# Performance work log

Hardware: AMD Instinct MI355X
Metric: run time of the kernel (lower is better)

## Reference

```python
import jax, jax.numpy as jnp
import numpy as np

B, NC, NF, D = 4, 256, 768, 768
TOK_RATIO = 0.5
LN_EPS = 1e-5


def _linear(x, w, b):
    # w: [D_in, D_out]
    return x @ w + b


def _leaky(x):
    return jax.nn.leaky_relu(x, negative_slope=0.01)


def setup_inputs() -> dict:
    key = jax.random.key(0)
    ks = jax.random.split(key, 12)
    s = 1.0 / np.sqrt(D)
    inp = {
        "cls_tokens": jax.random.normal(ks[0], (B, NC, D), dtype=jnp.float32),
        "feats": jax.random.normal(ks[1], (B, NF, D), dtype=jnp.float32),
        "W_head_w": jax.random.uniform(ks[2], (D, D), minval=-s, maxval=s),
        "W_head_b": jax.random.uniform(ks[3], (D,), minval=-s, maxval=s),
        "W_tail_w": jax.random.uniform(ks[4], (D, D), minval=-s, maxval=s),
        "W_tail_b": jax.random.uniform(ks[5], (D,), minval=-s, maxval=s),
        "lin1_w": jax.random.uniform(ks[6], (D, D), minval=-s, maxval=s),
        "lin1_b": jax.random.uniform(ks[7], (D,), minval=-s, maxval=s),
        "lin2_w": jax.random.uniform(ks[8], (D, D), minval=-s, maxval=s),
        "lin2_b": jax.random.uniform(ks[9], (D,), minval=-s, maxval=s),
        "ln_w": jnp.ones((D,), dtype=jnp.float32),
        "ln_b": jnp.zeros((D,), dtype=jnp.float32),
    }
    return inp


def reference(cls_tokens, feats, W_head_w, W_head_b, W_tail_w, W_tail_b,
              lin1_w, lin1_b, lin2_w, lin2_b, ln_w, ln_b):
    topk = int(TOK_RATIO * NC)
    scale = D ** (-0.5)

    # feats is detached in the original (clone().detach())
    x = jnp.concatenate([cls_tokens, jax.lax.stop_gradient(feats)], axis=1)  # [B, Nt, D]

    e_h = _linear(cls_tokens, W_head_w, W_head_b)  # [B, Nc, D]
    e_t = _linear(x, W_tail_w, W_tail_b)           # [B, Nt, D]

    attn_logit = jnp.einsum('bnd,bmd->bnm', e_h * scale, e_t)  # [B, Nc, Nt]
    topk_weight, topk_index = jax.lax.top_k(attn_logit, topk)  # [B, Nc, k]

    # Gather neighbor embeddings: Nb_h[b, n, j] = e_t[b, topk_index[b, n, j]]
    Nb_h = jax.vmap(lambda et, idx: et[idx])(e_t, topk_index)  # [B, Nc, k, D]

    topk_prob = jax.nn.softmax(topk_weight, axis=2)            # [B, Nc, k]
    p = topk_prob[..., None]
    eh_r = p * Nb_h + (1.0 - p) * e_h[:, :, None, :]           # [B, Nc, k, D]

    gate = jnp.tanh(e_h[:, :, None, :] + eh_r)
    ka_weight = jnp.einsum('bnkd,bnkd->bnk', Nb_h, gate)
    ka_prob = jax.nn.softmax(ka_weight, axis=2)
    e_Nh = jnp.einsum('bnk,bnkd->bnd', ka_prob, Nb_h)          # [B, Nc, D]

    # bi-interaction aggregation
    sum_emb = _leaky(_linear((e_h + e_Nh) * 0.1 + cls_tokens, lin1_w, lin1_b))
    bi_emb = _leaky(_linear(e_h * e_Nh * 0.1 + cls_tokens, lin2_w, lin2_b))
    embedding = sum_emb + bi_emb

    # LayerNorm (dropout is a no-op: p=0 and output overwritten in original)
    mu = jnp.mean(embedding, axis=-1, keepdims=True)
    var = jnp.var(embedding, axis=-1, keepdims=True)
    h = (embedding - mu) * jax.lax.rsqrt(var + LN_EPS) * ln_w + ln_b
    return h
```

## Files before the change

### kernel.cpp

```cpp
#include <hip/hip_runtime.h>
#include <hip/hip_bf16.h>
#include <math.h>

#define DDIM 768
#define NCLS 256
#define NFEAT 768
#define NTOK 1024
#define NBATCH 4
#define KSEL 128

typedef float f32x4 __attribute__((ext_vector_type(4)));
typedef short s16x8 __attribute__((ext_vector_type(8)));

__device__ __forceinline__ float wsum(float v) {
#pragma unroll
  for (int o = 32; o; o >>= 1) v += __shfl_down(v, o, 64);
  return v;
}
__device__ __forceinline__ float wmaxr(float v) {
#pragma unroll
  for (int o = 32; o; o >>= 1) v = fmaxf(v, __shfl_down(v, o, 64));
  return v;
}
__device__ __forceinline__ short f2bf(float f) {
  union { __hip_bfloat16 h; short s; } u;
  u.h = __float2bfloat16(f);
  return u.s;
}
__device__ __forceinline__ float bf2f(short s) {
  union { unsigned u; float f; } c;
  c.u = ((unsigned)(unsigned short)s) << 16;
  return c.f;
}
__device__ __forceinline__ void cvt8(float4 x, float4 y, s16x8& h, s16x8& l) {
  float v[8] = {x.x, x.y, x.z, x.w, y.x, y.y, y.z, y.w};
#pragma unroll
  for (int i = 0; i < 8; ++i) {
    short hh = f2bf(v[i]);
    h[i] = hh;
    l[i] = f2bf(v[i] - bf2f(hh));
  }
}

__global__ __launch_bounds__(256) void prep_weights(
    const float* __restrict__ w0, const float* __restrict__ w1,
    const float* __restrict__ w2, const float* __restrict__ w3,
    short* __restrict__ h0, short* __restrict__ h1, short* __restrict__ h2,
    short* __restrict__ h3, short* __restrict__ l0, short* __restrict__ l1) {
  __shared__ float tile[32][33];
  const int z = blockIdx.z;
  const float* s = z == 0 ? w0 : z == 1 ? w1 : z == 2 ? w2 : w3;
  short* dh = z == 0 ? h0 : z == 1 ? h1 : z == 2 ? h2 : h3;
  short* dl = z == 0 ? l0 : z == 1 ? l1 : nullptr;
  const int tx = threadIdx.x & 31, ty0 = threadIdx.x >> 5;
  const int r0 = blockIdx.y * 32, c0 = blockIdx.x * 32;
#pragma unroll
  for (int i = 0; i < 4; ++i) {
    int ty = ty0 + i * 8;
    tile[ty][tx] = s[(size_t)(r0 + ty) * DDIM + c0 + tx];
  }
  __syncthreads();
#pragma unroll
  for (int i = 0; i < 4; ++i) {
    int ty = ty0 + i * 8;
    float v = tile[tx][ty];
    short hh = f2bf(v);
    dh[(size_t)(c0 + ty) * DDIM + r0 + tx] = hh;
    if (dl) dl[(size_t)(c0 + ty) * DDIM + r0 + tx] = f2bf(v - bf2f(hh));
  }
}

__global__ __launch_bounds__(256) void gemm_front(
    const float* __restrict__ cls, const float* __restrict__ feats,
    const short* __restrict__ WhT_h, const short* __restrict__ WhT_l,
    const float* __restrict__ Whb, const short* __restrict__ WtT_h,
    const short* __restrict__ WtT_l, const float* __restrict__ Wtb,
    float* __restrict__ e_h, short* __restrict__ eh_hi,
    short* __restrict__ eh_lo, float* __restrict__ e_t,
    short* __restrict__ et_hi, short* __restrict__ et_lo) {
  __shared__ short Ah[64 * 40], Bh[64 * 40], Al[64 * 40], Bl[64 * 40];
  const int bid = blockIdx.x;
  const int xcd = bid & 7, idx = bid >> 3;
  const int ytile = xcd * 10 + idx / 12;
  const int xtile = idx % 12;
  const int t = threadIdx.x;
  const int row0 = ytile * 64;
  const int col0 = xtile * 64;
  const bool head = row0 < 1024;
  const int sr = t >> 2, sk = (t & 3) * 8;

  const float* aptr;
  {
    int gr = row0 + sr;
    if (head) {
      aptr = cls + (size_t)gr * DDIM;
    } else {
      int r2 = gr - 1024, b = r2 >> 10, rr = r2 & 1023;
      aptr = (rr < NCLS) ? (cls + ((size_t)b * NCLS + rr) * DDIM)
                         : (feats + ((size_t)b * NFEAT + (rr - NCLS)) * DDIM);
    }
    aptr += sk;
  }
  const short* bph = (head ? WhT_h : WtT_h) + (size_t)(col0 + sr) * DDIM + sk;
  const short* bpl = (head ? WhT_l : WtT_l) + (size_t)(col0 + sr) * DDIM + sk;
  const float* biasu = head ? Whb : Wtb;

  const int lane = t & 63, wave = t >> 6;
  const int wr = wave >> 1, wc = wave & 1;
  const int fr = lane & 15, fq = lane >> 4;

  f32x4 acc[2][2] = {};
  for (int k0 = 0; k0 < DDIM; k0 += 32) {
    float4 a0 = *(const float4*)(aptr + k0);
    float4 a1 = *(const float4*)(aptr + k0 + 4);
    s16x8 ah, al;
    cvt8(a0, a1, ah, al);
    s16x8 bh = *(const s16x8*)(bph + k0);
    s16x8 bl = *(const s16x8*)(bpl + k0);
    __syncthreads();
    *(s16x8*)&Ah[sr * 40 + sk] = ah;
    *(s16x8*)&Al[sr * 40 + sk] = al;
    *(s16x8*)&Bh[sr * 40 + sk] = bh;
    *(s16x8*)&Bl[sr * 40 + sk] = bl;
    __syncthreads();
#pragma unroll
    for (int n = 0; n < 2; ++n) {
      int bo = (wc * 32 + n * 16 + fr) * 40 + fq * 8;
      s16x8 bfh = *(const s16x8*)&Bh[bo];
      s16x8 bfl = *(const s16x8*)&Bl[bo];
#pragma unroll
      for (int m = 0; m < 2; ++m) {
        int ao = (wr * 32 + m * 16 + fr) * 40 + fq * 8;
        s16x8 afh = *(const s16x8*)&Ah[ao];
        s16x8 afl = *(const s16x8*)&Al[ao];
        acc[m][n] =
            __builtin_amdgcn_mfma_f32_16x16x32_bf16(afh, bfh, acc[m][n], 0, 0, 0);
        acc[m][n] =
            __builtin_amdgcn_mfma_f32_16x16x32_bf16(afh, bfl, acc[m][n], 0, 0, 0);
        acc[m][n] =
            __builtin_amdgcn_mfma_f32_16x16x32_bf16(afl, bfh, acc[m][n], 0, 0, 0);
      }
    }
  }

  float* Cf = head ? e_h : e_t;
  short* Ch = head ? eh_hi : et_hi;
  short* Cl = head ? eh_lo : et_lo;
  const int rbase = head ? row0 : row0 - 1024;
#pragma unroll
  for (int m = 0; m < 2; ++m) {
#pragma unroll
    for (int n = 0; n < 2; ++n) {
#pragma unroll
      for (int r = 0; r < 4; ++r) {
        int rg = rbase + wr * 32 + m * 16 + fq * 4 + r;
        int cg = col0 + wc * 32 + n * 16 + fr;
        float v = acc[m][n][r] + biasu[cg];
        size_t o = (size_t)rg * DDIM + cg;
        Cf[o] = v;
        short hh = f2bf(v);
        Ch[o] = hh;
        Cl[o] = f2bf(v - bf2f(hh));
      }
    }
  }
}

__global__ __launch_bounds__(256) void gemm_logits(
    const short* __restrict__ eh_hi, const short* __restrict__ eh_lo,
    const short* __restrict__ et_hi, const short* __restrict__ et_lo,
    float* __restrict__ logits, float scale) {
  __shared__ short Ah[32 * 40], Al[32 * 40], Bh[64 * 40], Bl[64 * 40];
  const int bid = blockIdx.x;
  const int xcd = bid & 7, idx = bid >> 3;
  const int batch = xcd >> 1;
  const int sub = ((xcd & 1) << 6) | idx;
  const int xtile = sub & 15, ytile = sub >> 4;
  const int row0 = ytile * 32, col0 = xtile * 64;
  const int t = threadIdx.x;

  const int ahalf = t >> 7, ac = t & 127;
  const int asr = ac >> 2, ask = (ac & 3) * 8;
  const short* aptr = (ahalf ? eh_lo : eh_hi) +
                      ((size_t)batch * NCLS + row0 + asr) * DDIM + ask;
  short* adst = (ahalf ? Al : Ah) + asr * 40 + ask;
  const int bsr = t >> 2, bsk = (t & 3) * 8;
  const short* bph = et_hi + ((size_t)batch * NTOK + col0 + bsr) * DDIM + bsk;
  const short* bpl = et_lo + ((size_t)batch * NTOK + col0 + bsr) * DDIM + bsk;
  short* bdh = Bh + bsr * 40 + bsk;
  short* bdl = Bl + bsr * 40 + bsk;

  const int lane = t & 63, wave = t >> 6;
  const int wr = wave >> 1, wc = wave & 1;
  const int fr = lane & 15, fq = lane >> 4;

  f32x4 acc[2] = {};
  for (int k0 = 0; k0 < DDIM; k0 += 32) {
    s16x8 av = *(const s16x8*)(aptr + k0);
    s16x8 bh = *(const s16x8*)(bph + k0);
    s16x8 bl = *(const s16x8*)(bpl + k0);
    __syncthreads();
    *(s16x8*)adst = av;
    *(s16x8*)bdh = bh;
    *(s16x8*)bdl = bl;
    __syncthreads();
    int ao = (wr * 16 + fr) * 40 + fq * 8;
    s16x8 afh = *(const s16x8*)&Ah[ao];
    s16x8 afl = *(const s16x8*)&Al[ao];
#pragma unroll
    for (int n = 0; n < 2; ++n) {
      int bo = (wc * 32 + n * 16 + fr) * 40 + fq * 8;
      s16x8 bfh = *(const s16x8*)&Bh[bo];
      s16x8 bfl = *(const s16x8*)&Bl[bo];
      acc[n] = __builtin_amdgcn_mfma_f32_16x16x32_bf16(afh, bfh, acc[n], 0, 0, 0);
      acc[n] = __builtin_amdgcn_mfma_f32_16x16x32_bf16(afh, bfl, acc[n], 0, 0, 0);
      acc[n] = __builtin_amdgcn_mfma_f32_16x16x32_bf16(afl, bfh, acc[n], 0, 0, 0);
    }
  }

  float* Cb = logits + (size_t)batch * NCLS * NTOK;
#pragma unroll
  for (int n = 0; n < 2; ++n)
#pragma unroll
    for (int r = 0; r < 4; ++r) {
      int rg = row0 + wr * 16 + fq * 4 + r;
      int cg = col0 + wc * 32 + n * 16 + fr;
      Cb[(size_t)rg * NTOK + cg] = scale * acc[n][r];
    }
}

__global__ __launch_bounds__(256) void gemm_lin(
    const short* __restrict__ inbf, const short* __restrict__ L1T,
    const short* __restrict__ L2T, const float* __restrict__ b1,
    const float* __restrict__ b2, float* __restrict__ C) {
  __shared__ short Ah[64 * 40], Bh[64 * 40];
  const int bid = blockIdx.x;
  const int xcd = bid & 7, idx = bid >> 3;
  const int ytile = xcd * 4 + idx / 12, xtile = idx % 12;
  const int t = threadIdx.x;
  const int row0 = ytile * 64, col0 = xtile * 64;
  const bool second = row0 >= 1024;
  const int sr = t >> 2, sk = (t & 3) * 8;
  const short* aptr = inbf + (size_t)(row0 + sr) * DDIM + sk;
  const short* bptr = (second ? L2T : L1T) + (size_t)(col0 + sr) * DDIM + sk;
  const float* biasu = second ? b2 : b1;
  const int lane = t & 63, wave = t >> 6;
  const int wr = wave >> 1, wc = wave & 1;
  const int fr = lane & 15, fq = lane >> 4;

  f32x4 acc[2][2] = {};
  for (int k0 = 0; k0 < DDIM; k0 += 32) {
    s16x8 ah = *(const s16x8*)(aptr + k0);
    s16x8 bh = *(const s16x8*)(bptr + k0);
    __syncthreads();
    *(s16x8*)&Ah[sr * 40 + sk] = ah;
    *(s16x8*)&Bh[sr * 40 + sk] = bh;
    __syncthreads();
#pragma unroll
    for (int n = 0; n < 2; ++n) {
      int bo = (wc * 32 + n * 16 + fr) * 40 + fq * 8;
      s16x8 bfh = *(const s16x8*)&Bh[bo];
#pragma unroll
      for (int m = 0; m < 2; ++m) {
        int ao = (wr * 32 + m * 16 + fr) * 40 + fq * 8;
        s16x8 afh = *(const s16x8*)&Ah[ao];
        acc[m][n] =
            __builtin_amdgcn_mfma_f32_16x16x32_bf16(afh, bfh, acc[m][n], 0, 0, 0);
      }
    }
  }
#pragma unroll
  for (int m = 0; m < 2; ++m)
#pragma unroll
    for (int n = 0; n < 2; ++n)
#pragma unroll
      for (int r = 0; r < 4; ++r) {
        int rg = row0 + wr * 32 + m * 16 + fq * 4 + r;
        int cg = col0 + wc * 32 + n * 16 + fr;
        float v = acc[m][n][r] + biasu[cg];
        v = v > 0.f ? v : 0.01f * v;
        C[(size_t)rg * DDIM + cg] = v;
      }
}

__global__ __launch_bounds__(256) void topk_select(
    const float* __restrict__ logits, float* __restrict__ tw,
    int* __restrict__ ti) {
  const int row = blockIdx.x;
  const int t = threadIdx.x;
  const int lane = t & 63, wave = t >> 6;
  __shared__ int hist[256];
  __shared__ int sh_bin, sh_rem;
  __shared__ int cnt;
  __shared__ int wsumT[4];

  float4 v4 = *(const float4*)(logits + (size_t)row * NTOK + 4 * t);
  float val[4] = {v4.x, v4.y, v4.z, v4.w};
  unsigned key[4];
#pragma unroll
  for (int i = 0; i < 4; ++i) {
    unsigned u = __float_as_uint(val[i]);
    key[i] = (u & 0x80000000u) ? ~u : (u | 0x80000000u);
  }

  unsigned pref = 0, mask = 0;
  int rem = KSEL;
#pragma unroll
  for (int shift = 24; shift >= 0; shift -= 8) {
    hist[t] = 0;
    __syncthreads();
#pragma unroll
    for (int i = 0; i < 4; ++i)
      if ((key[i] & mask) == pref)
        atomicAdd(&hist[(key[i] >> shift) & 255], 1);
    __syncthreads();
    if (wave == 0) {
      int h0 = hist[4 * lane], h1 = hist[4 * lane + 1];
      int h2 = hist[4 * lane + 2], h3 = hist[4 * lane + 3];
      int s = h0 + h1 + h2 + h3;
#pragma unroll
      for (int o = 1; o < 64; o <<= 1) {
        int v = __shfl_down(s, o, 64);
        if (lane + o < 64) s += v;
      }
      int abv = __shfl_down(s, 1, 64);
      if (lane == 63) abv = 0;
      int c3 = abv + h3, c2 = c3 + h2, c1 = c2 + h1, c0 = c1 + h0;
      int bin = -1, nab = 0;
      if (c3 >= rem && abv < rem) { bin = 4 * lane + 3; nab = abv; }
      else if (c2 >= rem && c3 < rem) { bin = 4 * lane + 2; nab = c3; }
      else if (c1 >= rem && c2 < rem) { bin = 4 * lane + 1; nab = c2; }
      else if (c0 >= rem && c1 < rem) { bin = 4 * lane + 0; nab = c1; }
      if (bin >= 0) { sh_bin = bin; sh_rem = rem - nab; }
    }
    __syncthreads();
    pref |= ((unsigned)sh_bin) << shift;
    mask |= 0xFFu << shift;
    rem = sh_rem;
  }

  const unsigned T = pref;
  const int above = KSEL - rem;

  if (t == 0) cnt = 0;
  int tc = 0;
#pragma unroll
  for (int i = 0; i < 4; ++i) tc += (key[i] == T);
  int inc = tc;
#pragma unroll
  for (int o = 1; o < 64; o <<= 1) {
    int v = __shfl_up(inc, o, 64);
    if (lane >= o) inc += v;
  }
  if (lane == 63) wsumT[wave] = inc;
  __syncthreads();
  int wbase = 0;
#pragma unroll
  for (int w = 0; w < 4; ++w)
    if (w < wave) wbase += wsumT[w];
  int excl = wbase + inc - tc;

  float* twr = tw + (size_t)row * KSEL;
  int* tir = ti + (size_t)row * KSEL;
#pragma unroll
  for (int i = 0; i < 4; ++i) {
    if (key[i] > T) {
      int slot = atomicAdd(&cnt, 1);
      twr[slot] = val[i];
      tir[slot] = 4 * t + i;
    } else if (key[i] == T) {
      int r = excl++;
      if (r < rem) {
        twr[above + r] = val[i];
        tir[above + r] = 4 * t + i;
      }
    }
  }
}

__global__ __launch_bounds__(256) void agg1(const float* __restrict__ e_h,
                                            const float* __restrict__ e_t,
                                            const float* __restrict__ tw,
                                            const int* __restrict__ ti,
                                            float* __restrict__ kaw_raw) {
  const int bid = blockIdx.x;
  const int xcd = bid & 7, slot = bid >> 3;
  const int batch = xcd >> 1;
  const int u = ((xcd & 1) << 8) | slot;
  const int row = batch * 256 + (u >> 1);
  const int half = u & 1;
  const int t = threadIdx.x, lane = t & 63, wave = t >> 6;
  __shared__ float p[KSEL];
  __shared__ int idxs[KSEL];
  __shared__ float red[2];

  if (t < KSEL) {
    p[t] = tw[(size_t)row * KSEL + t];
    idxs[t] = ti[(size_t)row * KSEL + t];
  }
  __syncthreads();
  if (wave == 0) {
    float m = wmaxr(fmaxf(p[lane], p[lane + 64]));
    if (!lane) red[0] = m;
  }
  __syncthreads();
  if (t < KSEL) p[t] = __expf(p[t] - red[0]);
  __syncthreads();
  if (wave == 0) {
    float s = wsum(p[lane] + p[lane + 64]);
    if (!lane) red[1] = s;
  }
  __syncthreads();
  if (t < KSEL) p[t] *= (1.f / red[1]);
  __syncthreads();

  float ehr[12];
  {
    const float* ehrow = e_h + (size_t)row * DDIM;
#pragma unroll
    for (int c = 0; c < 3; ++c) {
      float4 v = *(const float4*)(ehrow + 4 * lane + 256 * c);
      ehr[4 * c + 0] = v.x;
      ehr[4 * c + 1] = v.y;
      ehr[4 * c + 2] = v.z;
      ehr[4 * c + 3] = v.w;
    }
  }
  const float* etb = e_t + (size_t)batch * NTOK * DDIM;

  for (int i = 0; i < 16; ++i) {
    int j = half * 64 + wave * 16 + i;
    float pj = p[j];
    float a = 4.f - 2.f * pj, b2 = 2.f * pj;
    const float* nb = etb + (size_t)idxs[j] * DDIM;
    float partial = 0.f;
#pragma unroll
    for (int c = 0; c < 3; ++c) {
      float4 nv = *(const float4*)(nb + 4 * lane + 256 * c);
      float nq[4] = {nv.x, nv.y, nv.z, nv.w};
#pragma unroll
      for (int q = 0; q < 4; ++q) {
        float y2 = fmaf(a, ehr[4 * c + q], b2 * nq[q]);
        float ex = __expf(y2);
        float g = fmaf(-2.f, __builtin_amdgcn_rcpf(1.f + ex), 1.f);
        partial = fmaf(nq[q], g, partial);
      }
    }
    partial = wsum(partial);
    if (!lane) kaw_raw[(size_t)row * KSEL + j] = partial;
  }
}

__global__ __launch_bounds__(192) void agg2(
    const float* __restrict__ e_h, const float* __restrict__ e_t,
    const float* __restrict__ cls, const float* __restrict__ kaw_raw,
    const int* __restrict__ ti, short* __restrict__ inbf) {
  const int bid = blockIdx.x;
  const int xcd = bid & 7, slot = bid >> 3;
  const int batch = xcd >> 1;
  const int row = batch * 256 + (xcd & 1) * 128 + slot;
  const int t = threadIdx.x, lane = t & 63, wave = t >> 6;
  __shared__ float kp[KSEL];
  __shared__ int idxs[KSEL];
  __shared__ float red[2];

  if (t < KSEL) {
    kp[t] = kaw_raw[(size_t)row * KSEL + t];
    idxs[t] = ti[(size_t)row * KSEL + t];
  }
  __syncthreads();
  if (wave == 0) {
    float m = wmaxr(fmaxf(kp[lane], kp[lane + 64]));
    if (!lane) red[0] = m;
  }
  __syncthreads();
  if (t < KSEL) kp[t] = __expf(kp[t] - red[0]);
  __syncthreads();
  if (wave == 0) {
    float s = wsum(kp[lane] + kp[lane + 64]);
    if (!lane) red[1] = s;
  }
  __syncthreads();
  if (t < KSEL) kp[t] *= (1.f / red[1]);
  __syncthreads();

  const size_t o = (size_t)row * DDIM + 4 * t;
  float4 eh4 = *(const float4*)(e_h + o);
  float4 cl4 = *(const float4*)(cls + o);
  const float* etb = e_t + (size_t)batch * NTOK * DDIM;

  float ax = 0.f, ay = 0.f, az = 0.f, aw = 0.f;
#pragma unroll 8
  for (int j = 0; j < KSEL; ++j) {
    float pr = kp[j];
    float4 nb = *(const float4*)(etb + (size_t)idxs[j] * DDIM + 4 * t);
    ax = fmaf(pr, nb.x, ax);
    ay = fmaf(pr, nb.y, ay);
    az = fmaf(pr, nb.z, az);
    aw = fmaf(pr, nb.w, aw);
  }

  short4 sv, bv;
  sv.x = f2bf((eh4.x + ax) * 0.1f + cl4.x);
  sv.y = f2bf((eh4.y + ay) * 0.1f + cl4.y);
  sv.z = f2bf((eh4.z + az) * 0.1f + cl4.z);
  sv.w = f2bf((eh4.w + aw) * 0.1f + cl4.w);
  bv.x = f2bf((eh4.x * ax) * 0.1f + cl4.x);
  bv.y = f2bf((eh4.y * ay) * 0.1f + cl4.y);
  bv.z = f2bf((eh4.z * az) * 0.1f + cl4.z);
  bv.w = f2bf((eh4.w * aw) * 0.1f + cl4.w);
  *(short4*)&inbf[o] = sv;
  *(short4*)&inbf[(size_t)(NBATCH * NCLS) * DDIM + o] = bv;
}

__global__ __launch_bounds__(256) void ln_kernel(const float* __restrict__ embA,
                                                 const float* __restrict__ embB,
                                                 const float* __restrict__ lw,
                                                 const float* __restrict__ lb,
                                                 float* __restrict__ out) {
  const int row = blockIdx.x;
  const int t = threadIdx.x;
  const int lane = t & 63, wave = t >> 6;
  __shared__ float red[4];
  __shared__ float bs[2];
  float e[3];
#pragma unroll
  for (int c = 0; c < 3; ++c) {
    size_t o = (size_t)row * DDIM + t + 256 * c;
    e[c] = embA[o] + embB[o];
  }
  float s = e[0] + e[1] + e[2];
  s = wsum(s);
  if (lane == 0) red[wave] = s;
  __syncthreads();
  if (t == 0) bs[0] = (red[0] + red[1] + red[2] + red[3]) * (1.f / DDIM);
  __syncthreads();
  float mu = bs[0];
  float q = 0.f;
#pragma unroll
  for (int c = 0; c < 3; ++c) {
    float d = e[c] - mu;
    q = fmaf(d, d, q);
  }
  q = wsum(q);
  if (lane == 0) red[wave] = q;
  __syncthreads();
  if (t == 0) bs[1] = (red[0] + red[1] + red[2] + red[3]) * (1.f / DDIM);
  __syncthreads();
  float rstd = rsqrtf(bs[1] + 1e-5f);
#pragma unroll
  for (int c = 0; c < 3; ++c) {
    int d = t + 256 * c;
    out[(size_t)row * DDIM + d] = (e[c] - mu) * rstd * lw[d] + lb[d];
  }
}

extern "C" void kernel_launch(void* const* d_in, const int* in_sizes, int n_in,
                              void* d_out, int out_size, void* d_ws,
                              size_t ws_size, hipStream_t stream) {
  const float* cls = (const float*)d_in[0];
  const float* feats = (const float*)d_in[1];
  const float* Whw = (const float*)d_in[2];
  const float* Whb = (const float*)d_in[3];
  const float* Wtw = (const float*)d_in[4];
  const float* Wtb = (const float*)d_in[5];
  const float* l1w = (const float*)d_in[6];
  const float* l1b = (const float*)d_in[7];
  const float* l2w = (const float*)d_in[8];
  const float* l2b = (const float*)d_in[9];
  const float* lnw = (const float*)d_in[10];
  const float* lnb = (const float*)d_in[11];
  float* out = (float*)d_out;

  float* ws = (float*)d_ws;
  float* e_h = ws;
  float* e_t = ws + 786432;
  short* eh_hi = (short*)(ws + 3932160);
  short* eh_lo = eh_hi + 786432;
  short* et_hi = (short*)(ws + 4718592);
  short* et_lo = et_hi + 3145728;
  short* WhT_h = (short*)(ws + 7864320);
  short* WhT_l = WhT_h + 589824;
  short* WtT_h = WhT_h + 2 * 589824;
  short* WtT_l = WhT_h + 3 * 589824;
  short* L1T = (short*)(ws + 9043968);
  short* L2T = L1T + 589824;
  float* logits = ws + 7864320;
  float* tw = ws + 9633792;
  int* ti = (int*)(ws + 9764864);
  float* kaw = ws + 9895936;
  short* inbf = (short*)(ws + 10027008);
  float* linC = e_t;
  (void)ws_size;
  (void)in_sizes;
  (void)n_in;
  (void)out_size;

  const float scale = 0.036084391824351615f;
  dim3 blk(256);

  prep_weights<<<dim3(24, 24, 4), blk, 0, stream>>>(
      Whw, Wtw, l1w, l2w, WhT_h, WtT_h, L1T, L2T, WhT_l, WtT_l);
  gemm_front<<<dim3(960), blk, 0, stream>>>(
      cls, feats, WhT_h, WhT_l, Whb, WtT_h, WtT_l, Wtb, e_h, eh_hi, eh_lo, e_t,
      et_hi, et_lo);
  gemm_logits<<<dim3(512), blk, 0, stream>>>(eh_hi, eh_lo, et_hi, et_lo,
                                             logits, scale);
  topk_select<<<dim3(NBATCH * NCLS), blk, 0, stream>>>(logits, tw, ti);
  agg1<<<dim3(2048), blk, 0, stream>>>(e_h, e_t, tw, ti, kaw);
  agg2<<<dim3(1024), dim3(192), 0, stream>>>(e_h, e_t, cls, kaw, ti, inbf);
  gemm_lin<<<dim3(384), blk, 0, stream>>>(inbf, L1T, L2T, l1b, l2b, linC);
  ln_kernel<<<dim3(NBATCH * NCLS), blk, 0, stream>>>(
      linC, linC + (size_t)(NBATCH * NCLS) * DDIM, lnw, lnb, out);
}
```

Measured before the change: 130.9 us.

## Double-buffer LDS in GEMM kernels and pre-split activations to bf16 hi/lo

All three GEMM kernels now use two LDS buffers and load the next K-tile from global memory into registers while the current tile is consumed. This drops one barrier per iteration and hides global load latency behind the MFMA work. A new xprep kernel converts cls and feats once into bf16 hi/lo arrays, so gemm_front no longer repeats the fp32-to-bf16 split for every column tile. The cost is an extra launch, extra global traffic for the split copies, and doubled LDS use, which could lower occupancy.

```diff
diff --git a/kernel.cpp b/kernel.cpp
--- a/kernel.cpp
+++ b/kernel.cpp
@@ -40,6 +40,25 @@
     h[i] = hh;
     l[i] = f2bf(v[i] - bf2f(hh));
   }
+}
+
+__global__ __launch_bounds__(256) void xprep(const float* __restrict__ cls,
+                                             const float* __restrict__ feats,
+                                             short* __restrict__ Xh,
+                                             short* __restrict__ Xl) {
+  const size_t base = ((size_t)blockIdx.x * 256 + threadIdx.x) * 8;
+  const int row = (int)(base / DDIM);
+  const int col = (int)(base % DDIM);
+  const int b = row >> 10, rr = row & 1023;
+  const float* src = (rr < NCLS)
+                         ? cls + ((size_t)b * NCLS + rr) * DDIM + col
+                         : feats + ((size_t)b * NFEAT + (rr - NCLS)) * DDIM + col;
+  float4 a0 = *(const float4*)(src);
+  float4 a1 = *(const float4*)(src + 4);
+  s16x8 h, l;
+  cvt8(a0, a1, h, l);
+  *(s16x8*)(Xh + base) = h;
+  *(s16x8*)(Xl + base) = l;
 }
 
 __global__ __launch_bounds__(256) void prep_weights(
@@ -71,36 +90,28 @@
 }
 
 __global__ __launch_bounds__(256) void gemm_front(
-    const float* __restrict__ cls, const float* __restrict__ feats,
+    const short* __restrict__ Xh, const short* __restrict__ Xl,
     const short* __restrict__ WhT_h, const short* __restrict__ WhT_l,
     const float* __restrict__ Whb, const short* __restrict__ WtT_h,
     const short* __restrict__ WtT_l, const float* __restrict__ Wtb,
     float* __restrict__ e_h, short* __restrict__ eh_hi,
     short* __restrict__ eh_lo, float* __restrict__ e_t,
     short* __restrict__ et_hi, short* __restrict__ et_lo) {
-  __shared__ short Ah[64 * 40], Bh[64 * 40], Al[64 * 40], Bl[64 * 40];
+  __shared__ short Ah[2][64 * 40], Al[2][64 * 40];
+  __shared__ short Bh[2][64 * 40], Bl[2][64 * 40];
   const int bid = blockIdx.x;
   const int xcd = bid & 7, idx = bid >> 3;
   const int ytile = xcd * 10 + idx / 12;
   const int xtile = idx % 12;
   const int t = threadIdx.x;
-  const int row0 = ytile * 64;
-  const int col0 = xtile * 64;
+  const int row0 = ytile * 64, col0 = xtile * 64;
   const bool head = row0 < 1024;
   const int sr = t >> 2, sk = (t & 3) * 8;
 
-  const float* aptr;
-  {
-    int gr = row0 + sr;
-    if (head) {
-      aptr = cls + (size_t)gr * DDIM;
-    } else {
-      int r2 = gr - 1024, b = r2 >> 10, rr = r2 & 1023;
-      aptr = (rr < NCLS) ? (cls + ((size_t)b * NCLS + rr) * DDIM)
-                         : (feats + ((size_t)b * NFEAT + (rr - NCLS)) * DDIM);
-    }
-    aptr += sk;
-  }
+  size_t xrow = head ? (size_t)(((row0 >> 8) << 10) + (row0 & 255) + sr)
+                     : (size_t)(row0 - 1024 + sr);
+  const short* aph = Xh + xrow * DDIM + sk;
+  const short* apl = Xl + xrow * DDIM + sk;
   const short* bph = (head ? WhT_h : WtT_h) + (size_t)(col0 + sr) * DDIM + sk;
   const short* bpl = (head ? WhT_l : WtT_l) + (size_t)(col0 + sr) * DDIM + sk;
   const float* biasu = head ? Whb : Wtb;
@@ -108,31 +119,36 @@
   const int lane = t & 63, wave = t >> 6;
   const int wr = wave >> 1, wc = wave & 1;
   const int fr = lane & 15, fq = lane >> 4;
+  const int so = sr * 40 + sk;
 
   f32x4 acc[2][2] = {};
-  for (int k0 = 0; k0 < DDIM; k0 += 32) {
-    float4 a0 = *(const float4*)(aptr + k0);
-    float4 a1 = *(const float4*)(aptr + k0 + 4);
-    s16x8 ah, al;
-    cvt8(a0, a1, ah, al);
-    s16x8 bh = *(const s16x8*)(bph + k0);
-    s16x8 bl = *(const s16x8*)(bpl + k0);
+  s16x8 ra = *(const s16x8*)(aph);
+  s16x8 rla = *(const s16x8*)(apl);
+  s16x8 rb = *(const s16x8*)(bph);
+  s16x8 rlb = *(const s16x8*)(bpl);
+
+  for (int kt = 0; kt < 24; ++kt) {
+    const int cur = kt & 1;
+    *(s16x8*)&Ah[cur][so] = ra;
+    *(s16x8*)&Al[cur][so] = rla;
+    *(s16x8*)&Bh[cur][so] = rb;
+    *(s16x8*)&Bl[cur][so] = rlb;
     __syncthreads();
-    *(s16x8*)&Ah[sr * 40 + sk] = ah;
-    *(s16x8*)&Al[sr * 40 + sk] = al;
-    *(s16x8*)&Bh[sr * 40 + sk] = bh;
-    *(s16x8*)&Bl[sr * 40 + sk] = bl;
-    __syncthreads();
+    const int kn = (kt < 23 ? kt + 1 : 23) * 32;
+    ra = *(const s16x8*)(aph + kn);
+    rla = *(const s16x8*)(apl + kn);
+    rb = *(const s16x8*)(bph + kn);
+    rlb = *(const s16x8*)(bpl + kn);
 #pragma unroll
     for (int n = 0; n < 2; ++n) {
       int bo = (wc * 32 + n * 16 + fr) * 40 + fq * 8;
-      s16x8 bfh = *(const s16x8*)&Bh[bo];
-      s16x8 bfl = *(const s16x8*)&Bl[bo];
+      s16x8 bfh = *(const s16x8*)&Bh[cur][bo];
+      s16x8 bfl = *(const s16x8*)&Bl[cur][bo];
 #pragma unroll
       for (int m = 0; m < 2; ++m) {
         int ao = (wr * 32 + m * 16 + fr) * 40 + fq * 8;
-        s16x8 afh = *(const s16x8*)&Ah[ao];
-        s16x8 afl = *(const s16x8*)&Al[ao];
+        s16x8 afh = *(const s16x8*)&Ah[cur][ao];
+        s16x8 afl = *(const s16x8*)&Al[cur][ao];
         acc[m][n] =
             __builtin_amdgcn_mfma_f32_16x16x32_bf16(afh, bfh, acc[m][n], 0, 0, 0);
         acc[m][n] =
@@ -170,7 +186,8 @@
     const short* __restrict__ eh_hi, const short* __restrict__ eh_lo,
     const short* __restrict__ et_hi, const short* __restrict__ et_lo,
     float* __restrict__ logits, float scale) {
-  __shared__ short Ah[32 * 40], Al[32 * 40], Bh[64 * 40], Bl[64 * 40];
+  __shared__ short Ah[2][32 * 40], Al[2][32 * 40];
+  __shared__ short Bh[2][64 * 40], Bl[2][64 * 40];
   const int bid = blockIdx.x;
   const int xcd = bid & 7, idx = bid >> 3;
   const int batch = xcd >> 1;
@@ -183,35 +200,39 @@
   const int asr = ac >> 2, ask = (ac & 3) * 8;
   const short* aptr = (ahalf ? eh_lo : eh_hi) +
                       ((size_t)batch * NCLS + row0 + asr) * DDIM + ask;
-  short* adst = (ahalf ? Al : Ah) + asr * 40 + ask;
+  const int aso = asr * 40 + ask;
   const int bsr = t >> 2, bsk = (t & 3) * 8;
   const short* bph = et_hi + ((size_t)batch * NTOK + col0 + bsr) * DDIM + bsk;
   const short* bpl = et_lo + ((size_t)batch * NTOK + col0 + bsr) * DDIM + bsk;
-  short* bdh = Bh + bsr * 40 + bsk;
-  short* bdl = Bl + bsr * 40 + bsk;
+  const int bso = bsr * 40 + bsk;
 
   const int lane = t & 63, wave = t >> 6;
   const int wr = wave >> 1, wc = wave & 1;
   const int fr = lane & 15, fq = lane >> 4;
 
   f32x4 acc[2] = {};
-  for (int k0 = 0; k0 < DDIM; k0 += 32) {
-    s16x8 av = *(const s16x8*)(aptr + k0);
-    s16x8 bh = *(const s16x8*)(bph + k0);
-    s16x8 bl = *(const s16x8*)(bpl + k0);
+  s16x8 rA = *(const s16x8*)(aptr);
+  s16x8 rbh = *(const s16x8*)(bph);
+  s16x8 rbl = *(const s16x8*)(bpl);
+
+  for (int kt = 0; kt < 24; ++kt) {
+    const int cur = kt & 1;
+    *(s16x8*)&(ahalf ? Al : Ah)[cur][aso] = rA;
+    *(s16x8*)&Bh[cur][bso] = rbh;
+    *(s16x8*)&Bl[cur][bso] = rbl;
     __syncthreads();
-    *(s16x8*)adst = av;
-    *(s16x8*)bdh = bh;
-    *(s16x8*)bdl = bl;
-    __syncthreads();
+    const int kn = (kt < 23 ? kt + 1 : 23) * 32;
+    rA = *(const s16x8*)(aptr + kn);
+    rbh = *(const s16x8*)(bph + kn);
+    rbl = *(const s16x8*)(bpl + kn);
     int ao = (wr * 16 + fr) * 40 + fq * 8;
-    s16x8 afh = *(const s16x8*)&Ah[ao];
-    s16x8 afl = *(const s16x8*)&Al[ao];
+    s16x8 afh = *(const s16x8*)&Ah[cur][ao];
+    s16x8 afl = *(const s16x8*)&Al[cur][ao];
 #pragma unroll
     for (int n = 0; n < 2; ++n) {
       int bo = (wc * 32 + n * 16 + fr) * 40 + fq * 8;
-      s16x8 bfh = *(const s16x8*)&Bh[bo];
-      s16x8 bfl = *(const s16x8*)&Bl[bo];
+      s16x8 bfh = *(const s16x8*)&Bh[cur][bo];
+      s16x8 bfl = *(const s16x8*)&Bl[cur][bo];
       acc[n] = __builtin_amdgcn_mfma_f32_16x16x32_bf16(afh, bfh, acc[n], 0, 0, 0);
       acc[n] = __builtin_amdgcn_mfma_f32_16x16x32_bf16(afh, bfl, acc[n], 0, 0, 0);
       acc[n] = __builtin_amdgcn_mfma_f32_16x16x32_bf16(afl, bfh, acc[n], 0, 0, 0);
@@ -233,7 +254,7 @@
     const short* __restrict__ inbf, const short* __restrict__ L1T,
     const short* __restrict__ L2T, const float* __restrict__ b1,
     const float* __restrict__ b2, float* __restrict__ C) {
-  __shared__ short Ah[64 * 40], Bh[64 * 40];
+  __shared__ short Ah[2][64 * 40], Bh[2][64 * 40];
   const int bid = blockIdx.x;
   const int xcd = bid & 7, idx = bid >> 3;
   const int ytile = xcd * 4 + idx / 12, xtile = idx % 12;
@@ -247,23 +268,27 @@
   const int lane = t & 63, wave = t >> 6;
   const int wr = wave >> 1, wc = wave & 1;
   const int fr = lane & 15, fq = lane >> 4;
+  const int so = sr * 40 + sk;
 
   f32x4 acc[2][2] = {};
-  for (int k0 = 0; k0 < DDIM; k0 += 32) {
-    s16x8 ah = *(const s16x8*)(aptr + k0);
-    s16x8 bh = *(const s16x8*)(bptr + k0);
+  s16x8 rA = *(const s16x8*)(aptr);
+  s16x8 rB = *(const s16x8*)(bptr);
+  for (int kt = 0; kt < 24; ++kt) {
+    const int cur = kt & 1;
+    *(s16x8*)&Ah[cur][so] = rA;
+    *(s16x8*)&Bh[cur][so] = rB;
     __syncthreads();
-    *(s16x8*)&Ah[sr * 40 + sk] = ah;
-    *(s16x8*)&Bh[sr * 40 + sk] = bh;
-    __syncthreads();
+    const int kn = (kt < 23 ? kt + 1 : 23) * 32;
+    rA = *(const s16x8*)(aptr + kn);
+    rB = *(const s16x8*)(bptr + kn);
 #pragma unroll
     for (int n = 0; n < 2; ++n) {
       int bo = (wc * 32 + n * 16 + fr) * 40 + fq * 8;
-      s16x8 bfh = *(const s16x8*)&Bh[bo];
+      s16x8 bfh = *(const s16x8*)&Bh[cur][bo];
 #pragma unroll
       for (int m = 0; m < 2; ++m) {
         int ao = (wr * 32 + m * 16 + fr) * 40 + fq * 8;
-        s16x8 afh = *(const s16x8*)&Ah[ao];
+        s16x8 afh = *(const s16x8*)&Ah[cur][ao];
         acc[m][n] =
             __builtin_amdgcn_mfma_f32_16x16x32_bf16(afh, bfh, acc[m][n], 0, 0, 0);
       }
@@ -586,6 +611,8 @@
   short* L1T = (short*)(ws + 9043968);
   short* L2T = L1T + 589824;
   float* logits = ws + 7864320;
+  short* Xh = (short*)(ws + 9633792);
+  short* Xl = Xh + 3145728;
   float* tw = ws + 9633792;
   int* ti = (int*)(ws + 9764864);
   float* kaw = ws + 9895936;
@@ -599,10 +626,11 @@
   const float scale = 0.036084391824351615f;
   dim3 blk(256);
 
+  xprep<<<dim3(1536), blk, 0, stream>>>(cls, feats, Xh, Xl);
   prep_weights<<<dim3(24, 24, 4), blk, 0, stream>>>(
       Whw, Wtw, l1w, l2w, WhT_h, WtT_h, L1T, L2T, WhT_l, WtT_l);
   gemm_front<<<dim3(960), blk, 0, stream>>>(
-      cls, feats, WhT_h, WhT_l, Whb, WtT_h, WtT_l, Wtb, e_h, eh_hi, eh_lo, e_t,
+      Xh, Xl, WhT_h, WhT_l, Whb, WtT_h, WtT_l, Wtb, e_h, eh_hi, eh_lo, e_t,
       et_hi, et_lo);
   gemm_logits<<<dim3(512), blk, 0, stream>>>(eh_hi, eh_lo, et_hi, et_lo,
                                              logits, scale);
```

Result: slower. 137.4 us (+4.9%).
